# Kernel optimization log

Measured on AMD Instinct MI355X. Metric: run time of the kernel, lower is better.

Reference implementation:

```python
import jax, jax.numpy as jnp
import numpy as np
import math

DIM = 1536
HEADS = 4
DIM_KEY = 64
DIM_VALUE = 64
NUM_REL_POS_FEATURES = 64
SEQ_LEN = 4096  # must match the hard-coded positional buffer seq_len in the torch module
SCALE = DIM_KEY ** -0.5


def positional_embed(seq_len, feature_size):
    # get_positional_embed: central-mask features + sign-antisymmetric copy
    distances = jnp.arange(-seq_len + 1, seq_len)  # (2n-1,)
    nb = feature_size // 2  # one feature fn, 2 components
    pow_rate = math.exp(math.log(seq_len + 1) / nb)
    center_widths = jnp.power(jnp.float32(pow_rate), jnp.arange(1, nb + 1, dtype=jnp.float32)) - 1.0
    emb = (center_widths[None, :] > jnp.abs(distances)[:, None]).astype(jnp.float32)  # (2n-1, nb)
    sign = jnp.sign(distances).astype(jnp.float32)[:, None]
    return jnp.concatenate([emb, sign * emb], axis=-1)  # (2n-1, feature_size)


def setup_inputs() -> dict:
    key = jax.random.key(0)
    ks = jax.random.split(key, 9)
    b, n, dim, h, dk, dv, F = 1, SEQ_LEN, DIM, HEADS, DIM_KEY, DIM_VALUE, NUM_REL_POS_FEATURES
    s = 0.02
    x = jax.random.normal(ks[0], (b, n, dim), dtype=jnp.float32)
    Wq = jax.random.normal(ks[1], (dim, h * dk), dtype=jnp.float32) * s
    Wk = jax.random.normal(ks[2], (dim, h * dk), dtype=jnp.float32) * s
    Wv = jax.random.normal(ks[3], (dim, h * dv), dtype=jnp.float32) * s
    W_rel_k = jax.random.normal(ks[4], (F, h * dk), dtype=jnp.float32) * s
    Wo = jax.random.normal(ks[5], (h * dv, dim), dtype=jnp.float32) * s  # torch inits zeros; random for a meaningful test
    bo = jnp.zeros((dim,), dtype=jnp.float32)
    rel_content_bias = jax.random.normal(ks[6], (1, h, 1, dk), dtype=jnp.float32)
    rel_pos_bias = jax.random.normal(ks[7], (1, h, 1, dk), dtype=jnp.float32)
    return {"x": x, "Wq": Wq, "Wk": Wk, "Wv": Wv, "W_rel_k": W_rel_k, "Wo": Wo, "bo": bo,
            "rel_content_bias": rel_content_bias, "rel_pos_bias": rel_pos_bias}


def reference(x, Wq, Wk, Wv, W_rel_k, Wo, bo, rel_content_bias, rel_pos_bias):
    b, n, _ = x.shape
    h, dk, dv = HEADS, DIM_KEY, DIM_VALUE
    # projections -> (b, h, n, d)
    q = (x @ Wq).reshape(b, n, h, dk).transpose(0, 2, 1, 3) * SCALE
    k = (x @ Wk).reshape(b, n, h, dk).transpose(0, 2, 1, 3)
    v = (x @ Wv).reshape(b, n, h, dv).transpose(0, 2, 1, 3)
    # content logits with content bias
    content_logits = jnp.einsum('bhid,bhjd->bhij', q + rel_content_bias, k)
    # relative-position keys from fixed positional buffer (pos_dropout p=0 -> identity)
    positions = positional_embed(SEQ_LEN, NUM_REL_POS_FEATURES)  # (2n-1, F)
    rel_k = (positions @ W_rel_k).reshape(2 * n - 1, h, dk).transpose(1, 0, 2)  # (h, 2n-1, dk)
    # rel logits then Transformer-XL strided shift: rel_logits[i, j] = r[i, n-1 + j - i]
    r = jnp.einsum('bhid,hjd->bhij', q + rel_pos_bias, rel_k)  # (b, h, n, 2n-1)
    idx = (n - 1) + jnp.arange(n)[None, :] - jnp.arange(n)[:, None]  # (n, n)
    rel_logits = jnp.take_along_axis(r, jnp.broadcast_to(idx[None, None], (b, h, n, n)), axis=-1)
    attn = jax.nn.softmax(content_logits + rel_logits, axis=-1)  # attn_dropout p=0 -> identity
    out = jnp.einsum('bhij,bhjd->bhid', attn, v)
    out = out.transpose(0, 2, 1, 3).reshape(b, n, h * dv)
    return out @ Wo + bo
```

## Files before the change

kernel.cpp:

```cpp
#include <hip/hip_runtime.h>
#include <hip/hip_bf16.h>

#define N_SEQ 4096
#define DIMM  1536
#define NH    4
#define DK    64
#define HD    256
#define QK_SCALE 0.125f
#define WSZ   393216
#define KSPLIT 8
#define LOG2E 1.44269504f

typedef __bf16 bf16x8 __attribute__((ext_vector_type(8)));
typedef unsigned short u16;
typedef u16   u16x8  __attribute__((ext_vector_type(8)));
typedef u16   u16x4  __attribute__((ext_vector_type(4)));
typedef float f32x4  __attribute__((ext_vector_type(4)));
typedef float f32x16 __attribute__((ext_vector_type(16)));
typedef unsigned int u32x4 __attribute__((ext_vector_type(4)));

__device__ inline float b2f(u16 u){
    union { float f; unsigned int i; } v; v.i = ((unsigned int)u) << 16; return v.f;
}
__device__ inline u16 f2b(float f){
    __bf16 h = (__bf16)f;
    return __builtin_bit_cast(u16, h);
}
__device__ inline bf16x8 ldfrag(const u16* p){
    return __builtin_bit_cast(bf16x8, *(const u16x8*)p);
}
__device__ inline f32x16 zero16(){
    f32x16 v;
    #pragma unroll
    for (int i = 0; i < 16; ++i) v[i] = 0.f;
    return v;
}
#define EXP2(x) exp2f(x)

__global__ __launch_bounds__(256) void convwt_kernel(const float* __restrict__ Wq,
    const float* __restrict__ Wk, const float* __restrict__ Wv, u16* __restrict__ Wt){
    __shared__ float T[64 * 65];
    int bid = blockIdx.x;
    int s = bid / 96, tile = bid % 96;
    int n0 = (tile / 24) * 64;
    int k0 = (tile % 24) * 64;
    const float* W = (s == 0) ? Wq : (s == 1 ? Wk : Wv);
    int t = threadIdx.x;
    int rA = t >> 3, c8 = (t & 7) * 8;
    #pragma unroll
    for (int rep = 0; rep < 2; ++rep){
        int rr = rep * 32 + rA;
        const float* p = W + (size_t)(k0 + rr) * HD + n0 + c8;
        f32x4 a = *(const f32x4*)p, b = *(const f32x4*)(p + 4);
        #pragma unroll
        for (int e = 0; e < 4; ++e){
            T[rr * 65 + c8 + e]     = a[e];
            T[rr * 65 + c8 + 4 + e] = b[e];
        }
    }
    __syncthreads();
    #pragma unroll
    for (int rep = 0; rep < 2; ++rep){
        int rn = rep * 32 + rA;
        u16x8 o;
        #pragma unroll
        for (int e = 0; e < 8; ++e) o[e] = f2b(T[(c8 + e) * 65 + rn]);
        *(u16x8*)&Wt[(size_t)s * WSZ + (size_t)(n0 + rn) * DIMM + k0 + c8] = o;
    }
}

__global__ __launch_bounds__(256) void fmtab_kernel(unsigned char* __restrict__ fmt,
    const float* __restrict__ Wrel, u16* __restrict__ WsP, u16* __restrict__ WsM){
    int t = threadIdx.x;
    if (blockIdx.x == 16){
        int h = t >> 6, d = t & 63;
        float w1[32], w2[32];
        #pragma unroll
        for (int fm = 0; fm < 32; ++fm){
            w1[fm] = Wrel[(size_t)fm * HD + h * DK + d];
            w2[fm] = Wrel[(size_t)(32 + fm) * HD + h * DK + d];
        }
        float a1 = 0.f, a2 = 0.f;
        #pragma unroll
        for (int fm = 31; fm >= 0; --fm){
            a1 += w1[fm];
            a2 += w2[fm];
            WsP[(h * 32 + fm) * 64 + d] = f2b(a1 + a2);
            WsM[(h * 32 + fm) * 64 + d] = f2b(a1 - a2);
        }
        return;
    }
    int d = blockIdx.x * 256 + t;
    float lg = logf((float)(N_SEQ + 1)) * (1.0f / 32.0f);
    float ad = (float)d;
    int fm = 0;
    for (int f = 0; f < 32; ++f){
        float cw = expf(lg * (float)(f + 1)) - 1.0f;
        fm += (cw <= ad) ? 1 : 0;
    }
    fmt[d] = (unsigned char)fm;
}

__global__ __launch_bounds__(256) void qkv_kernel(const float* __restrict__ X,
    const u16* __restrict__ Wt,
    u16* __restrict__ Q, u16* __restrict__ K, u16* __restrict__ Vt){
    __shared__ __align__(16) u16 xs[64 * 72];
    __shared__ __align__(16) u16 bs[64 * 72];
    int s  = blockIdx.x >> 2;
    int n0 = (blockIdx.x & 3) * 64;
    int m0 = blockIdx.y * 64;
    int t = threadIdx.x;
    int w = t >> 6, lane = t & 63, qd = lane >> 4, l15 = lane & 15;
    int r  = t >> 3;
    int cv = (t & 7) * 8;
    f32x4 acc[4] = {{0,0,0,0},{0,0,0,0},{0,0,0,0},{0,0,0,0}};

    f32x4 xa[2], xb[2];
    u16x8 wv[2];
    auto LOAD = [&](int k0){
        #pragma unroll
        for (int rep = 0; rep < 2; ++rep){
            int rr = rep * 32 + r;
            size_t xi = (size_t)(m0 + rr) * DIMM + k0 + cv;
            xa[rep] = *(const f32x4*)(X + xi);
            xb[rep] = *(const f32x4*)(X + xi + 4);
            wv[rep] = *(const u16x8*)&Wt[(size_t)s * WSZ + (size_t)(n0 + rr) * DIMM + k0 + cv];
        }
    };
    auto STORE = [&](){
        #pragma unroll
        for (int rep = 0; rep < 2; ++rep){
            int rr = rep * 32 + r;
            u16x8 xv;
            #pragma unroll
            for (int e = 0; e < 4; ++e){ xv[e] = f2b(xa[rep][e]); xv[4 + e] = f2b(xb[rep][e]); }
            *(u16x8*)&xs[rr * 72 + cv] = xv;
            *(u16x8*)&bs[rr * 72 + cv] = wv[rep];
        }
    };

    LOAD(0);
    for (int k0 = 0; k0 < DIMM; k0 += 64){
        STORE();
        __syncthreads();
        if (k0 + 64 < DIMM) LOAD(k0 + 64);
        bf16x8 a0 = ldfrag(&xs[(w * 16 + l15) * 72 +  0 + qd * 8]);
        bf16x8 a1 = ldfrag(&xs[(w * 16 + l15) * 72 + 32 + qd * 8]);
        #pragma unroll
        for (int nt = 0; nt < 4; ++nt){
            bf16x8 b0 = ldfrag(&bs[(nt * 16 + l15) * 72 +  0 + qd * 8]);
            bf16x8 b1 = ldfrag(&bs[(nt * 16 + l15) * 72 + 32 + qd * 8]);
            acc[nt] = __builtin_amdgcn_mfma_f32_16x16x32_bf16(a0, b0, acc[nt], 0, 0, 0);
            acc[nt] = __builtin_amdgcn_mfma_f32_16x16x32_bf16(a1, b1, acc[nt], 0, 0, 0);
        }
        __syncthreads();
    }

    int row0 = m0 + w * 16 + qd * 4;
    if (s == 0){
        #pragma unroll
        for (int nt = 0; nt < 4; ++nt){
            int col = n0 + nt * 16 + l15;
            #pragma unroll
            for (int reg = 0; reg < 4; ++reg)
                Q[(size_t)(row0 + reg) * HD + col] = f2b(acc[nt][reg] * QK_SCALE);
        }
    } else if (s == 1){
        #pragma unroll
        for (int nt = 0; nt < 4; ++nt){
            int col = n0 + nt * 16 + l15;
            #pragma unroll
            for (int reg = 0; reg < 4; ++reg)
                K[(size_t)(row0 + reg) * HD + col] = f2b(acc[nt][reg]);
        }
    } else {
        #pragma unroll
        for (int nt = 0; nt < 4; ++nt){
            int col = n0 + nt * 16 + l15;
            u16x4 pv;
            #pragma unroll
            for (int reg = 0; reg < 4; ++reg) pv[reg] = f2b(acc[nt][reg]);
            *(u16x4*)&Vt[(size_t)col * N_SEQ + row0] = pv;
        }
    }
}

__global__ __launch_bounds__(256) void attn_kernel(const u16* __restrict__ Q,
    const u16* __restrict__ Kg, const u16* __restrict__ Vt,
    const u16* __restrict__ WsPg, const u16* __restrict__ WsMg,
    const unsigned char* __restrict__ fmtg,
    const float* __restrict__ CB, const float* __restrict__ PB,
    u16* __restrict__ OpU, float* __restrict__ mpart, float* __restrict__ lpart){
    __shared__ __align__(16) unsigned char smem[39936];
    u16* Ks   = (u16*)(smem);
    u16* Vts  = (u16*)(smem + 9216);
    u16* Qs   = (u16*)(smem);
    u16* relP = (u16*)(smem + 18432);
    u16* relM = (u16*)(smem + 27136);
    unsigned char* fmt = smem + 35840;
    u16* WsPs = (u16*)(smem + 18432);
    u16* WsMs = (u16*)(smem + 23040);

    int i0   = blockIdx.x * 128;
    int h    = blockIdx.y;
    int half = blockIdx.z;
    int bid  = blockIdx.x * NH + h;
    int jbase = half * (N_SEQ / KSPLIT);
    const int NT = (N_SEQ / KSPLIT) / 64;
    int t = threadIdx.x;
    int w = t >> 6, lane = t & 63, l31 = lane & 31, hbit = lane >> 5;
    int h8 = hbit * 8;
    int i_loc = w * 32 + l31;

    int sr = t >> 3, scv = (t & 7) * 8;
    u16x8 kr0, kr1, vr0, vr1;
    auto LOAD = [&](int j0){
        kr0 = *(const u16x8*)&Kg[(size_t)(j0 + sr)      * HD + h * DK + scv];
        kr1 = *(const u16x8*)&Kg[(size_t)(j0 + 32 + sr) * HD + h * DK + scv];
        vr0 = *(const u16x8*)&Vt[(size_t)(h * 64 + sr)      * N_SEQ + j0 + scv];
        vr1 = *(const u16x8*)&Vt[(size_t)(h * 64 + 32 + sr) * N_SEQ + j0 + scv];
    };
    auto STORE = [&](){
        *(u16x8*)&Ks [(sr)      * 72 + scv] = kr0;
        *(u16x8*)&Ks [(32 + sr) * 72 + scv] = kr1;
        *(u16x8*)&Vts[(sr)      * 72 + scv] = vr0;
        *(u16x8*)&Vts[(32 + sr) * 72 + scv] = vr1;
    };
    LOAD(jbase);

    #pragma unroll
    for (int rep = 0; rep < 4; ++rep){
        int vid = rep * 256 + t;
        int r  = vid >> 3;
        int cv = (vid & 7) * 8;
        *(u16x8*)&Qs[r * 72 + cv] = *(const u16x8*)&Q[(size_t)(i0 + r) * HD + h * DK + cv];
    }
    {
        int r = t >> 3, cv = (t & 7) * 8;
        *(u16x8*)&WsPs[r * 72 + cv] = *(const u16x8*)&WsPg[(h * 32 + r) * 64 + cv];
        *(u16x8*)&WsMs[r * 72 + cv] = *(const u16x8*)&WsMg[(h * 32 + r) * 64 + cv];
    }
    ((uint4*)fmt)[t] = ((const uint4*)fmtg)[t];
    __syncthreads();

    bf16x8 qcF[4], qpF[4];
    #pragma unroll
    for (int kc = 0; kc < 4; ++kc){
        bf16x8 raw = ldfrag(&Qs[i_loc * 72 + kc * 16 + h8]);
        const float* cbp = CB + h * DK + kc * 16 + h8;
        const float* pbp = PB + h * DK + kc * 16 + h8;
        bf16x8 qc, qp;
        #pragma unroll
        for (int e = 0; e < 8; ++e){
            float qf = (float)raw[e];
            qc[e] = (__bf16)((qf + cbp[e]) * LOG2E);
            qp[e] = (__bf16)((qf + pbp[e]) * LOG2E);
        }
        qcF[kc] = qc; qpF[kc] = qp;
    }

    f32x16 rP = zero16(), rM = zero16();
    #pragma unroll
    for (int kc = 0; kc < 4; ++kc){
        bf16x8 aP = ldfrag(&WsPs[l31 * 72 + kc * 16 + h8]);
        bf16x8 aM = ldfrag(&WsMs[l31 * 72 + kc * 16 + h8]);
        rP = __builtin_amdgcn_mfma_f32_32x32x16_bf16(aP, qpF[kc], rP, 0, 0, 0);
        rM = __builtin_amdgcn_mfma_f32_32x32x16_bf16(aM, qpF[kc], rM, 0, 0, 0);
    }
    __syncthreads();

    #pragma unroll
    for (int r = 0; r < 16; ++r){
        int fm = (r & 3) + 8 * (r >> 2) + 4 * hbit;
        relP[i_loc * 34 + fm] = f2b(rP[r]);
        relM[i_loc * 34 + fm] = f2b(rM[r]);
    }
    if (hbit == 0)
        relP[i_loc * 34 + 0] = f2b((rP[0] + rM[0]) * 0.5f);
    STORE();
    __syncthreads();

    float mrow = -1e30f, lacc = 0.f;
    f32x16 oacc0 = zero16(), oacc1 = zero16();

#define MFMA32(A, B, C) __builtin_amdgcn_mfma_f32_32x32x16_bf16(A, B, C, 0, 0, 0)

#define PACK8(ST, WD) { \
    _Pragma("unroll") \
    for (int q_ = 0; q_ < 8; ++q_){ \
        float pa_ = EXP2(ST[2 * q_]     - bias); \
        float pc_ = EXP2(ST[2 * q_ + 1] - bias); \
        lsum += pa_ + pc_; \
        WD[q_] = (unsigned int)f2b(pa_) | ((unsigned int)f2b(pc_) << 16); \
    } }

#define MKFRAG(DST, WD, ZZ) { \
    unsigned int a0_ = WD[(ZZ) * 4 + 0], a1_ = WD[(ZZ) * 4 + 1]; \
    unsigned int b0_ = WD[(ZZ) * 4 + 2], b1_ = WD[(ZZ) * 4 + 3]; \
    unsigned int sh0_ = (unsigned int)__shfl_xor((int)(hbit ? a0_ : b0_), 32); \
    unsigned int sh1_ = (unsigned int)__shfl_xor((int)(hbit ? a1_ : b1_), 32); \
    u32x4 fw_; \
    fw_[0] = hbit ? sh0_ : a0_; \
    fw_[1] = hbit ? sh1_ : a1_; \
    fw_[2] = hbit ? b0_  : sh0_; \
    fw_[3] = hbit ? b1_  : sh1_; \
    DST = __builtin_bit_cast(bf16x8, fw_); }

#define PVSTEP(PF, COL) { \
    oacc0 = MFMA32(PF, ldfrag(&Vts[(l31)      * 72 + (COL) + h8]), oacc0); \
    oacc1 = MFMA32(PF, ldfrag(&Vts[(32 + l31) * 72 + (COL) + h8]), oacc1); }

    const u16* relP_i = relP + i_loc * 34;
    const u16* relM_i = relM + i_loc * 34;

    for (int kt = 0; kt < NT; ++kt){
        int j0 = jbase + kt * 64;
        if (kt + 1 < NT) LOAD(j0 + 64);

        f32x16 st0 = zero16(), st1 = zero16();
        __builtin_amdgcn_s_setprio(1);
        #pragma unroll
        for (int kc = 0; kc < 4; ++kc){
            bf16x8 k0 = ldfrag(&Ks[(l31)      * 72 + kc * 16 + h8]);
            bf16x8 k1 = ldfrag(&Ks[(32 + l31) * 72 + kc * 16 + h8]);
            st0 = MFMA32(k0, qcF[kc], st0);
            st1 = MFMA32(k1, qcF[kc], st1);
        }
        __builtin_amdgcn_s_setprio(0);

        int D = j0 - i0;
        int Di = D - i_loc;
        float relv = 0.f;
        bool fast = false; int fmU = 0; const u16* tabU = relP_i;
        if (D >= 128){
            int fa = fmt[D - 127], fb = fmt[D + 63];
            fast = (fa == fb); fmU = fa; tabU = relP_i;
        } else if (D <= -64){
            int fa = fmt[-D - 63], fb = fmt[-D + 127];
            fast = (fa == fb); fmU = fa; tabU = relM_i;
        }
        if (fast){
            relv = b2f(tabU[fmU]);
        } else {
            #pragma unroll
            for (int r = 0; r < 16; ++r){
                const int jb = (r & 3) + 8 * (r >> 2);
                int jbh = jb + 4 * hbit;
                {
                    int dd = Di + jbh;
                    int ad = dd < 0 ? -dd : dd;
                    int fm = fmt[ad];
                    const u16* tab = (dd >= 0) ? relP_i : relM_i;
                    st0[r] += b2f(tab[fm]);
                }
                {
                    int dd = Di + 32 + jbh;
                    int ad = dd < 0 ? -dd : dd;
                    int fm = fmt[ad];
                    const u16* tab = (dd >= 0) ? relP_i : relM_i;
                    st1[r] += b2f(tab[fm]);
                }
            }
        }

        float mx = st0[0];
        #pragma unroll
        for (int r = 1; r < 16; ++r) mx = fmaxf(mx, st0[r]);
        #pragma unroll
        for (int r = 0; r < 16; ++r) mx = fmaxf(mx, st1[r]);
        mx = fmaxf(mx, __shfl_xor(mx, 32)) + relv;

        if (!__all(mx - mrow <= 11.0f)){
            float mnew = fmaxf(mrow, mx);
            float alpha = EXP2(mrow - mnew);
            mrow = mnew;
            lacc *= alpha;
            #pragma unroll
            for (int r = 0; r < 16; ++r){
                float ar = __shfl(alpha, (r & 3) + 8 * (r >> 2) + 4 * hbit);
                oacc0[r] *= ar; oacc1[r] *= ar;
            }
        }

        float bias = mrow - relv;
        float lsum = 0.f;
        unsigned int wds0[8], wds1[8];
        PACK8(st0, wds0)
        PACK8(st1, wds1)
        lacc += lsum + __shfl_xor(lsum, 32);

        bf16x8 pf0, pf1, pf2, pf3;
        MKFRAG(pf0, wds0, 0)
        MKFRAG(pf1, wds0, 1)
        MKFRAG(pf2, wds1, 0)
        MKFRAG(pf3, wds1, 1)
        __builtin_amdgcn_s_setprio(1);
        PVSTEP(pf0,  0)
        PVSTEP(pf1, 16)
        PVSTEP(pf2, 32)
        PVSTEP(pf3, 48)
        __builtin_amdgcn_s_setprio(0);

        __syncthreads();
        if (kt + 1 < NT) STORE();
        __syncthreads();
    }

    size_t pb = ((size_t)half * 128 + bid) * 128;
    #pragma unroll
    for (int r = 0; r < 16; ++r){
        int iO = w * 32 + (r & 3) + 8 * (r >> 2) + 4 * hbit;
        OpU[(pb + iO) * 64 + l31]      = f2b(oacc0[r]);
        OpU[(pb + iO) * 64 + 32 + l31] = f2b(oacc1[r]);
    }
    if (hbit == 0){
        mpart[pb + i_loc] = mrow;
        lpart[pb + i_loc] = lacc;
    }
#undef MFMA32
#undef PACK8
#undef MKFRAG
#undef PVSTEP
}

__global__ __launch_bounds__(256) void combine_kernel(const u16* __restrict__ OpU,
    const float* __restrict__ mpart, const float* __restrict__ lpart,
    u16* __restrict__ Oatt){
    int h = blockIdx.y;
    int t = threadIdx.x;
    int r = t >> 3, cb = (t & 7) * 8;
    int i = blockIdx.x * 32 + r;
    int bid = (i >> 7) * NH + h;
    int ri = i & 127;
    size_t pr[8];
    float ms[8], ls[8];
    float m = -1e30f;
    #pragma unroll
    for (int s = 0; s < 8; ++s){
        pr[s] = ((size_t)s * 128 + bid) * 128 + ri;
        ms[s] = mpart[pr[s]];
        ls[s] = lpart[pr[s]];
        m = fmaxf(m, ms[s]);
    }
    float den = 0.f, wgt[8];
    #pragma unroll
    for (int s = 0; s < 8; ++s){ wgt[s] = EXP2(ms[s] - m); den += wgt[s] * ls[s]; }
    float inv = 1.0f / fmaxf(den, 1e-30f);
    float o[8];
    #pragma unroll
    for (int e = 0; e < 8; ++e) o[e] = 0.f;
    #pragma unroll
    for (int s = 0; s < 8; ++s){
        u16x8 a = *(const u16x8*)&OpU[pr[s] * 64 + cb];
        #pragma unroll
        for (int e = 0; e < 8; ++e) o[e] += wgt[s] * b2f(a[e]);
    }
    u16x8 rv;
    #pragma unroll
    for (int e = 0; e < 8; ++e) rv[e] = f2b(o[e] * inv);
    *(u16x8*)&Oatt[(size_t)i * HD + h * DK + cb] = rv;
}

__global__ __launch_bounds__(256) void oproj_kernel(const u16* __restrict__ A,
    const float* __restrict__ Wo, const float* __restrict__ bo,
    float* __restrict__ out, int m_base){
    __shared__ __align__(16) u16 xs[64 * 72];
    __shared__ __align__(16) u16 bs[64 * 72];
    int m0 = m_base + blockIdx.y * 64;
    int n0 = blockIdx.x * 64;
    int t = threadIdx.x;
    int w = t >> 6, lane = t & 63, qd = lane >> 4, l15 = lane & 15;
    f32x4 acc[4] = {{0,0,0,0},{0,0,0,0},{0,0,0,0},{0,0,0,0}};
    for (int k0 = 0; k0 < HD; k0 += 64){
        #pragma unroll
        for (int rep = 0; rep < 2; ++rep){
            int vid = rep * 256 + t;
            int r  = vid >> 3;
            int cv = (vid & 7) * 8;
            *(u16x8*)&xs[r * 72 + cv] = *(const u16x8*)&A[(size_t)(m0 + r) * HD + k0 + cv];
            size_t wi = (size_t)(k0 + r) * DIMM + n0 + cv;
            f32x4 wa = *(const f32x4*)(Wo + wi), wb = *(const f32x4*)(Wo + wi + 4);
            u16x8 wv;
            #pragma unroll
            for (int e = 0; e < 4; ++e){ wv[e] = f2b(wa[e]); wv[4 + e] = f2b(wb[e]); }
            #pragma unroll
            for (int e = 0; e < 8; ++e) bs[(cv + e) * 72 + r] = wv[e];
        }
        __syncthreads();
        bf16x8 a0 = ldfrag(&xs[(w * 16 + l15) * 72 +  0 + qd * 8]);
        bf16x8 a1 = ldfrag(&xs[(w * 16 + l15) * 72 + 32 + qd * 8]);
        #pragma unroll
        for (int nt = 0; nt < 4; ++nt){
            bf16x8 b0 = ldfrag(&bs[(nt * 16 + l15) * 72 +  0 + qd * 8]);
            bf16x8 b1 = ldfrag(&bs[(nt * 16 + l15) * 72 + 32 + qd * 8]);
            acc[nt] = __builtin_amdgcn_mfma_f32_16x16x32_bf16(a0, b0, acc[nt], 0, 0, 0);
            acc[nt] = __builtin_amdgcn_mfma_f32_16x16x32_bf16(a1, b1, acc[nt], 0, 0, 0);
        }
        __syncthreads();
    }
    #pragma unroll
    for (int nt = 0; nt < 4; ++nt)
        #pragma unroll
        for (int reg = 0; reg < 4; ++reg){
            int row = m0 + w * 16 + qd * 4 + reg;
            int col = n0 + nt * 16 + l15;
            out[(size_t)row * DIMM + col] = acc[nt][reg] + bo[col];
        }
}

extern "C" void kernel_launch(void* const* d_in, const int* in_sizes, int n_in,
                              void* d_out, int out_size, void* d_ws, size_t ws_size,
                              hipStream_t stream){
    const float* X  = (const float*)d_in[0];
    const float* Wq = (const float*)d_in[1];
    const float* Wk = (const float*)d_in[2];
    const float* Wv = (const float*)d_in[3];
    const float* Wr = (const float*)d_in[4];
    const float* Wo = (const float*)d_in[5];
    const float* bo = (const float*)d_in[6];
    const float* CB = (const float*)d_in[7];
    const float* PB = (const float*)d_in[8];
    float* out = (float*)d_out;
    u16* base = (u16*)d_out;

    u16* Qb   = base;
    u16* Kb   = base + 1048576;
    u16* Vt   = base + 2097152;
    u16* Wt   = base + 3145728;
    u16* OpU  = base + 3145728;
    float* mpart = out + 5767168;
    float* lpart = out + 5898240;
    u16* Oatt = base;

    unsigned char* fmtg = (unsigned char*)d_ws;
    u16* WsP = (u16*)((char*)d_ws + 4096);
    u16* WsM = (u16*)((char*)d_ws + 20480);

    convwt_kernel<<<dim3(288), 256, 0, stream>>>(Wq, Wk, Wv, Wt);
    fmtab_kernel<<<dim3(17), 256, 0, stream>>>(fmtg, Wr, WsP, WsM);
    qkv_kernel<<<dim3(12, 64), 256, 0, stream>>>(X, Wt, Qb, Kb, Vt);
    attn_kernel<<<dim3(32, NH, KSPLIT), 256, 0, stream>>>(Qb, Kb, Vt, WsP, WsM,
                                                          fmtg, CB, PB,
                                                          OpU, mpart, lpart);
    combine_kernel<<<dim3(128, NH), 256, 0, stream>>>(OpU, mpart, lpart, Oatt);

    oproj_kernel<<<dim3(24, 58), 256, 0, stream>>>(Oatt, Wo, bo, out, 384);
    oproj_kernel<<<dim3(24,  5), 256, 0, stream>>>(Oatt, Wo, bo, out, 64);
    oproj_kernel<<<dim3(24,  1), 256, 0, stream>>>(Oatt, Wo, bo, out, 0);
}
```

Baseline: 223.3 us.

## Double-buffer K/V tiles in attention, move rel table to global, merge prep kernels

```diff
diff --git a/kernel.cpp b/kernel.cpp
--- a/kernel.cpp
+++ b/kernel.cpp
@@ -13,6 +13,7 @@
 
 typedef __bf16 bf16x8 __attribute__((ext_vector_type(8)));
 typedef unsigned short u16;
+typedef unsigned int u32;
 typedef u16   u16x8  __attribute__((ext_vector_type(8)));
 typedef u16   u16x4  __attribute__((ext_vector_type(4)));
 typedef float f32x4  __attribute__((ext_vector_type(4)));
@@ -37,42 +38,42 @@
 }
 #define EXP2(x) exp2f(x)
 
-__global__ __launch_bounds__(256) void convwt_kernel(const float* __restrict__ Wq,
-    const float* __restrict__ Wk, const float* __restrict__ Wv, u16* __restrict__ Wt){
-    __shared__ float T[64 * 65];
+__global__ __launch_bounds__(256) void prep_kernel(const float* __restrict__ Wq,
+    const float* __restrict__ Wk, const float* __restrict__ Wv, u16* __restrict__ Wt,
+    unsigned char* __restrict__ fmt, const float* __restrict__ Wrel,
+    u16* __restrict__ WsP, u16* __restrict__ WsM){
     int bid = blockIdx.x;
-    int s = bid / 96, tile = bid % 96;
-    int n0 = (tile / 24) * 64;
-    int k0 = (tile % 24) * 64;
-    const float* W = (s == 0) ? Wq : (s == 1 ? Wk : Wv);
     int t = threadIdx.x;
-    int rA = t >> 3, c8 = (t & 7) * 8;
-    #pragma unroll
-    for (int rep = 0; rep < 2; ++rep){
-        int rr = rep * 32 + rA;
-        const float* p = W + (size_t)(k0 + rr) * HD + n0 + c8;
-        f32x4 a = *(const f32x4*)p, b = *(const f32x4*)(p + 4);
-        #pragma unroll
-        for (int e = 0; e < 4; ++e){
-            T[rr * 65 + c8 + e]     = a[e];
-            T[rr * 65 + c8 + 4 + e] = b[e];
-        }
-    }
-    __syncthreads();
-    #pragma unroll
-    for (int rep = 0; rep < 2; ++rep){
-        int rn = rep * 32 + rA;
-        u16x8 o;
-        #pragma unroll
-        for (int e = 0; e < 8; ++e) o[e] = f2b(T[(c8 + e) * 65 + rn]);
-        *(u16x8*)&Wt[(size_t)s * WSZ + (size_t)(n0 + rn) * DIMM + k0 + c8] = o;
-    }
-}
-
-__global__ __launch_bounds__(256) void fmtab_kernel(unsigned char* __restrict__ fmt,
-    const float* __restrict__ Wrel, u16* __restrict__ WsP, u16* __restrict__ WsM){
-    int t = threadIdx.x;
-    if (blockIdx.x == 16){
+    if (bid < 288){
+        __shared__ float T[64 * 65];
+        int s = bid / 96, tile = bid % 96;
+        int n0 = (tile / 24) * 64;
+        int k0 = (tile % 24) * 64;
+        const float* W = (s == 0) ? Wq : (s == 1 ? Wk : Wv);
+        int rA = t >> 3, c8 = (t & 7) * 8;
+        #pragma unroll
+        for (int rep = 0; rep < 2; ++rep){
+            int rr = rep * 32 + rA;
+            const float* p = W + (size_t)(k0 + rr) * HD + n0 + c8;
+            f32x4 a = *(const f32x4*)p, b = *(const f32x4*)(p + 4);
+            #pragma unroll
+            for (int e = 0; e < 4; ++e){
+                T[rr * 65 + c8 + e]     = a[e];
+                T[rr * 65 + c8 + 4 + e] = b[e];
+            }
+        }
+        __syncthreads();
+        #pragma unroll
+        for (int rep = 0; rep < 2; ++rep){
+            int rn = rep * 32 + rA;
+            u16x8 o;
+            #pragma unroll
+            for (int e = 0; e < 8; ++e) o[e] = f2b(T[(c8 + e) * 65 + rn]);
+            *(u16x8*)&Wt[(size_t)s * WSZ + (size_t)(n0 + rn) * DIMM + k0 + c8] = o;
+        }
+        return;
+    }
+    if (bid == 304){
         int h = t >> 6, d = t & 63;
         float w1[32], w2[32];
         #pragma unroll
@@ -90,7 +91,7 @@
         }
         return;
     }
-    int d = blockIdx.x * 256 + t;
+    int d = (bid - 288) * 256 + t;
     float lg = logf((float)(N_SEQ + 1)) * (1.0f / 32.0f);
     float ad = (float)d;
     int fm = 0;
@@ -185,19 +186,18 @@
     }
 }
 
-__global__ __launch_bounds__(256) void attn_kernel(const u16* __restrict__ Q,
+template<bool RELG>
+__global__ __launch_bounds__(256, 4) void attn_kernel(const u16* __restrict__ Q,
     const u16* __restrict__ Kg, const u16* __restrict__ Vt,
     const u16* __restrict__ WsPg, const u16* __restrict__ WsMg,
     const unsigned char* __restrict__ fmtg,
     const float* __restrict__ CB, const float* __restrict__ PB,
+    u32* __restrict__ relG,
     u16* __restrict__ OpU, float* __restrict__ mpart, float* __restrict__ lpart){
-    __shared__ __align__(16) unsigned char smem[39936];
-    u16* Ks   = (u16*)(smem);
-    u16* Vts  = (u16*)(smem + 9216);
+    extern __shared__ __align__(16) unsigned char smem[];
+    unsigned char* fmt = smem + 36864;
+    u32* relL = (u32*)(smem + 40960);
     u16* Qs   = (u16*)(smem);
-    u16* relP = (u16*)(smem + 18432);
-    u16* relM = (u16*)(smem + 27136);
-    unsigned char* fmt = smem + 35840;
     u16* WsPs = (u16*)(smem + 18432);
     u16* WsMs = (u16*)(smem + 23040);
 
@@ -220,11 +220,13 @@
         vr0 = *(const u16x8*)&Vt[(size_t)(h * 64 + sr)      * N_SEQ + j0 + scv];
         vr1 = *(const u16x8*)&Vt[(size_t)(h * 64 + 32 + sr) * N_SEQ + j0 + scv];
     };
-    auto STORE = [&](){
-        *(u16x8*)&Ks [(sr)      * 72 + scv] = kr0;
-        *(u16x8*)&Ks [(32 + sr) * 72 + scv] = kr1;
-        *(u16x8*)&Vts[(sr)      * 72 + scv] = vr0;
-        *(u16x8*)&Vts[(32 + sr) * 72 + scv] = vr1;
+    auto STOREB = [&](int b){
+        u16* Kb = (u16*)(smem + b * 18432);
+        u16* Vb = Kb + 4608;
+        *(u16x8*)&Kb[(sr)      * 72 + scv] = kr0;
+        *(u16x8*)&Kb[(32 + sr) * 72 + scv] = kr1;
+        *(u16x8*)&Vb[(sr)      * 72 + scv] = vr0;
+        *(u16x8*)&Vb[(32 + sr) * 72 + scv] = vr1;
     };
     LOAD(jbase);
 
@@ -269,15 +271,21 @@
     }
     __syncthreads();
 
-    #pragma unroll
-    for (int r = 0; r < 16; ++r){
-        int fm = (r & 3) + 8 * (r >> 2) + 4 * hbit;
-        relP[i_loc * 34 + fm] = f2b(rP[r]);
-        relM[i_loc * 34 + fm] = f2b(rM[r]);
-    }
-    if (hbit == 0)
-        relP[i_loc * 34 + 0] = f2b((rP[0] + rM[0]) * 0.5f);
-    STORE();
+    u32* relRow;
+    if (RELG) relRow = relG + ((size_t)h * N_SEQ + (size_t)(i0 + i_loc)) * 32;
+    else      relRow = relL + i_loc * 32;
+    {
+        u32 v0 = (u32)f2b((rP[0] + rM[0]) * 0.5f);
+        u32 v0p = v0 | (v0 << 16);
+        #pragma unroll
+        for (int r = 0; r < 16; ++r){
+            int fm = (r & 3) + 8 * (r >> 2) + 4 * hbit;
+            u32 pk = (u32)f2b(rP[r]) | ((u32)f2b(rM[r]) << 16);
+            relRow[fm] = (fm == 0) ? v0p : pk;
+        }
+    }
+    STOREB(0);
+    LOAD(jbase + 64);
     __syncthreads();
 
     float mrow = -1e30f, lacc = 0.f;
@@ -291,14 +299,14 @@
         float pa_ = EXP2(ST[2 * q_]     - bias); \
         float pc_ = EXP2(ST[2 * q_ + 1] - bias); \
         lsum += pa_ + pc_; \
-        WD[q_] = (unsigned int)f2b(pa_) | ((unsigned int)f2b(pc_) << 16); \
+        WD[q_] = (u32)f2b(pa_) | ((u32)f2b(pc_) << 16); \
     } }
 
 #define MKFRAG(DST, WD, ZZ) { \
-    unsigned int a0_ = WD[(ZZ) * 4 + 0], a1_ = WD[(ZZ) * 4 + 1]; \
-    unsigned int b0_ = WD[(ZZ) * 4 + 2], b1_ = WD[(ZZ) * 4 + 3]; \
-    unsigned int sh0_ = (unsigned int)__shfl_xor((int)(hbit ? a0_ : b0_), 32); \
-    unsigned int sh1_ = (unsigned int)__shfl_xor((int)(hbit ? a1_ : b1_), 32); \
+    u32 a0_ = WD[(ZZ) * 4 + 0], a1_ = WD[(ZZ) * 4 + 1]; \
+    u32 b0_ = WD[(ZZ) * 4 + 2], b1_ = WD[(ZZ) * 4 + 3]; \
+    u32 sh0_ = (u32)__shfl_xor((int)(hbit ? a0_ : b0_), 32); \
+    u32 sh1_ = (u32)__shfl_xor((int)(hbit ? a1_ : b1_), 32); \
     u32x4 fw_; \
     fw_[0] = hbit ? sh0_ : a0_; \
     fw_[1] = hbit ? sh1_ : a1_; \
@@ -307,22 +315,23 @@
     DST = __builtin_bit_cast(bf16x8, fw_); }
 
 #define PVSTEP(PF, COL) { \
-    oacc0 = MFMA32(PF, ldfrag(&Vts[(l31)      * 72 + (COL) + h8]), oacc0); \
-    oacc1 = MFMA32(PF, ldfrag(&Vts[(32 + l31) * 72 + (COL) + h8]), oacc1); }
-
-    const u16* relP_i = relP + i_loc * 34;
-    const u16* relM_i = relM + i_loc * 34;
+    oacc0 = MFMA32(PF, ldfrag(&Vcur[(l31)      * 72 + (COL) + h8]), oacc0); \
+    oacc1 = MFMA32(PF, ldfrag(&Vcur[(32 + l31) * 72 + (COL) + h8]), oacc1); }
 
     for (int kt = 0; kt < NT; ++kt){
+        int cur = kt & 1;
         int j0 = jbase + kt * 64;
-        if (kt + 1 < NT) LOAD(j0 + 64);
+        if (kt + 1 < NT) STOREB(cur ^ 1);
+        if (kt + 2 < NT) LOAD(j0 + 128);
+        const u16* Kcur = (const u16*)(smem + cur * 18432);
+        const u16* Vcur = Kcur + 4608;
 
         f32x16 st0 = zero16(), st1 = zero16();
         __builtin_amdgcn_s_setprio(1);
         #pragma unroll
         for (int kc = 0; kc < 4; ++kc){
-            bf16x8 k0 = ldfrag(&Ks[(l31)      * 72 + kc * 16 + h8]);
-            bf16x8 k1 = ldfrag(&Ks[(32 + l31) * 72 + kc * 16 + h8]);
+            bf16x8 k0 = ldfrag(&Kcur[(l31)      * 72 + kc * 16 + h8]);
+            bf16x8 k1 = ldfrag(&Kcur[(32 + l31) * 72 + kc * 16 + h8]);
             st0 = MFMA32(k0, qcF[kc], st0);
             st1 = MFMA32(k1, qcF[kc], st1);
         }
@@ -331,16 +340,17 @@
         int D = j0 - i0;
         int Di = D - i_loc;
         float relv = 0.f;
-        bool fast = false; int fmU = 0; const u16* tabU = relP_i;
+        bool fast = false, plus = true; int fmU = 0;
         if (D >= 128){
             int fa = fmt[D - 127], fb = fmt[D + 63];
-            fast = (fa == fb); fmU = fa; tabU = relP_i;
+            fast = (fa == fb); fmU = fa; plus = true;
         } else if (D <= -64){
             int fa = fmt[-D - 63], fb = fmt[-D + 127];
-            fast = (fa == fb); fmU = fa; tabU = relM_i;
+            fast = (fa == fb); fmU = fa; plus = false;
         }
         if (fast){
-            relv = b2f(tabU[fmU]);
+            u32 pm = relRow[fmU];
+            relv = b2f(plus ? (u16)pm : (u16)(pm >> 16));
         } else {
             #pragma unroll
             for (int r = 0; r < 16; ++r){
@@ -349,16 +359,14 @@
                 {
                     int dd = Di + jbh;
                     int ad = dd < 0 ? -dd : dd;
-                    int fm = fmt[ad];
-                    const u16* tab = (dd >= 0) ? relP_i : relM_i;
-                    st0[r] += b2f(tab[fm]);
+                    u32 pm = relRow[fmt[ad]];
+                    st0[r] += b2f(dd >= 0 ? (u16)pm : (u16)(pm >> 16));
                 }
                 {
                     int dd = Di + 32 + jbh;
                     int ad = dd < 0 ? -dd : dd;
-                    int fm = fmt[ad];
-                    const u16* tab = (dd >= 0) ? relP_i : relM_i;
-                    st1[r] += b2f(tab[fm]);
+                    u32 pm = relRow[fmt[ad]];
+                    st1[r] += b2f(dd >= 0 ? (u16)pm : (u16)(pm >> 16));
                 }
             }
         }
@@ -384,7 +392,7 @@
 
         float bias = mrow - relv;
         float lsum = 0.f;
-        unsigned int wds0[8], wds1[8];
+        u32 wds0[8], wds1[8];
         PACK8(st0, wds0)
         PACK8(st1, wds1)
         lacc += lsum + __shfl_xor(lsum, 32);
@@ -401,8 +409,6 @@
         PVSTEP(pf3, 48)
         __builtin_amdgcn_s_setprio(0);
 
-        __syncthreads();
-        if (kt + 1 < NT) STORE();
         __syncthreads();
     }
 
@@ -530,21 +536,29 @@
     u16* OpU  = base + 3145728;
     float* mpart = out + 5767168;
     float* lpart = out + 5898240;
-    u16* Oatt = base;
 
     unsigned char* fmtg = (unsigned char*)d_ws;
     u16* WsP = (u16*)((char*)d_ws + 4096);
     u16* WsM = (u16*)((char*)d_ws + 20480);
-
-    convwt_kernel<<<dim3(288), 256, 0, stream>>>(Wq, Wk, Wv, Wt);
-    fmtab_kernel<<<dim3(17), 256, 0, stream>>>(fmtg, Wr, WsP, WsM);
+    u32* relG = (u32*)((char*)d_ws + 36864);
+    bool ws_ok = ws_size >= 4231168;
+
+    prep_kernel<<<dim3(305), 256, 0, stream>>>(Wq, Wk, Wv, Wt, fmtg, Wr, WsP, WsM);
     qkv_kernel<<<dim3(12, 64), 256, 0, stream>>>(X, Wt, Qb, Kb, Vt);
-    attn_kernel<<<dim3(32, NH, KSPLIT), 256, 0, stream>>>(Qb, Kb, Vt, WsP, WsM,
-                                                          fmtg, CB, PB,
-                                                          OpU, mpart, lpart);
-    combine_kernel<<<dim3(128, NH), 256, 0, stream>>>(OpU, mpart, lpart, Oatt);
-
-    oproj_kernel<<<dim3(24, 58), 256, 0, stream>>>(Oatt, Wo, bo, out, 384);
-    oproj_kernel<<<dim3(24,  5), 256, 0, stream>>>(Oatt, Wo, bo, out, 64);
-    oproj_kernel<<<dim3(24,  1), 256, 0, stream>>>(Oatt, Wo, bo, out, 0);
-}
+
+    if (ws_ok){
+        u16* Oatt = (u16*)((char*)d_ws + 2134016);
+        attn_kernel<true><<<dim3(32, NH, KSPLIT), 256, 40960, stream>>>(
+            Qb, Kb, Vt, WsP, WsM, fmtg, CB, PB, relG, OpU, mpart, lpart);
+        combine_kernel<<<dim3(128, NH), 256, 0, stream>>>(OpU, mpart, lpart, Oatt);
+        oproj_kernel<<<dim3(24, 64), 256, 0, stream>>>(Oatt, Wo, bo, out, 0);
+    } else {
+        u16* Oatt = base;
+        attn_kernel<false><<<dim3(32, NH, KSPLIT), 256, 57344, stream>>>(
+            Qb, Kb, Vt, WsP, WsM, fmtg, CB, PB, nullptr, OpU, mpart, lpart);
+        combine_kernel<<<dim3(128, NH), 256, 0, stream>>>(OpU, mpart, lpart, Oatt);
+        oproj_kernel<<<dim3(24, 58), 256, 0, stream>>>(Oatt, Wo, bo, out, 384);
+        oproj_kernel<<<dim3(24,  5), 256, 0, stream>>>(Oatt, Wo, bo, out, 64);
+        oproj_kernel<<<dim3(24,  1), 256, 0, stream>>>(Oatt, Wo, bo, out, 0);
+    }
+}
```

After: 433.8 us. 94.3% more time.
